# Performance work log

Hardware: AMD Instinct MI355X
Metric: run time of the kernel (lower is better)

Reference implementation:

```python
import jax, jax.numpy as jnp
import numpy as np
from jax import lax

RADIUS = 5


def setup_inputs() -> dict:
    key = jax.random.key(0)
    k1, k2 = jax.random.split(key)
    B, K, H, W = 4, 6, 128, 128
    win = 2 * RADIUS + 1
    labels = jax.random.uniform(k1, (B, K, H, W), dtype=jnp.float32)
    weights = jax.random.uniform(k2, (B, H * W, win, win), dtype=jnp.float32)
    return {"labels": labels, "weights": weights}


def reference(labels, weights):
    # labels:  [B, K, H, W]  class probabilities
    B, K, H, W = labels.shape
    win = 2 * RADIUS + 1
    N = H * W

    # Extract 11x11 patches around every pixel for all classes at once.
    patches = lax.conv_general_dilated_patches(
        labels, (win, win), (1, 1), padding=[(RADIUS, RADIUS), (RADIUS, RADIUS)]
    )
    patches = patches.reshape(B, K, win * win, N)

    w = weights.reshape(B, N, win * win)

    # sum over window of weights * P, per class: wp[b,k,n] = sum_o w[b,n,o] * patches[b,k,o,n]
    wp = jnp.einsum('bkon,bno->bkn', patches, w)

    p = labels.reshape(B, K, N)
    num = jnp.einsum('bkn,bkn->bk', p, wp)          # association
    den = jnp.einsum('bkn,bn->bk', p, w.sum(-1))    # degree
    L = num / den                                    # [B, K]

    # nn.L1Loss()(L, zeros) per class = mean_b |L[b,k]|
    losses = jnp.mean(jnp.abs(L), axis=0)            # [K]
    return K - jnp.sum(losses)
```

## Files before the change

kernel.cpp:

```cpp
#include <hip/hip_runtime.h>

#define RADIUS 5
#define WIN    11
#define WIN2   121
#define KCLS   6
#define HH     128
#define WW     128
#define BB     4
#define NPIX   (HH*WW)
#define TPB    256
#define NBLK   (BB*HH*2)
#define PXB    64
#define LABW   (PXB + 2*RADIUS)
#define NSITE  (WIN*LABW)
#define PLSTR  (NSITE*2)

__global__ __launch_bounds__(TPB, 4) void ncut_main(
    const float* __restrict__ labels,
    const float* __restrict__ weights,
    float* __restrict__ part) {
  __shared__ float shl[3 * PLSTR];
  __shared__ float shred[4 * 12];

  const int tid = threadIdx.x;
  const int blk = blockIdx.x;
  const int b   = blk >> 8;
  const int rem = blk & 255;
  const int y0  = rem >> 1;
  const int x0  = (rem & 1) * PXB;

  const float* labB = labels + (size_t)b * KCLS * NPIX;
  for (int s = tid; s < NSITE; s += TPB) {
    const int tr = s / LABW;
    const int tc = s - tr * LABW;
    const int gy = y0 - RADIUS + tr;
    const int gx = x0 + tc - RADIUS;
    const bool ok = ((unsigned)gy < (unsigned)HH) & ((unsigned)gx < (unsigned)WW);
    const float* lp = labB + (size_t)gy * WW + gx;
#pragma unroll
    for (int p = 0; p < 3; ++p) {
      float2 v = make_float2(0.f, 0.f);
      if (ok) {
        v.x = lp[(size_t)(2 * p) * NPIX];
        v.y = lp[(size_t)(2 * p + 1) * NPIX];
      }
      *reinterpret_cast<float2*>(shl + p * PLSTR + 2 * s) = v;
    }
  }
  __syncthreads();

  const int px = tid >> 2;
  const int q  = tid & 3;
  const float* wrowq = weights +
      ((size_t)b * NPIX + (size_t)y0 * WW + x0 + px) * WIN2 + q;

  float2 a0 = make_float2(0.f, 0.f);
  float2 a1 = make_float2(0.f, 0.f);
  float2 a2 = make_float2(0.f, 0.f);
  float wsum = 0.f;

#pragma unroll
  for (int j = 0; j < 30; ++j) {
    const int o4 = 4 * j;
    const int S  = (o4 / WIN) * LABW + (o4 % WIN);
    const int Wn = WIN - (o4 % WIN);
    const float w = wrowq[o4];
    wsum += w;
    int li = px + S + q;
    if (Wn < 4) li += (q >= Wn) ? (LABW - WIN) : 0;
    const float2 v0 = *reinterpret_cast<const float2*>(shl + 0 * PLSTR + 2 * li);
    const float2 v1 = *reinterpret_cast<const float2*>(shl + 1 * PLSTR + 2 * li);
    const float2 v2 = *reinterpret_cast<const float2*>(shl + 2 * PLSTR + 2 * li);
    a0.x += w * v0.x; a0.y += w * v0.y;
    a1.x += w * v1.x; a1.y += w * v1.y;
    a2.x += w * v2.x; a2.y += w * v2.y;
  }
  if (q == 0) {
    const float w = wrowq[120];
    const int li = px + 10 * LABW + 10;
    wsum += w;
    const float2 v0 = *reinterpret_cast<const float2*>(shl + 0 * PLSTR + 2 * li);
    const float2 v1 = *reinterpret_cast<const float2*>(shl + 1 * PLSTR + 2 * li);
    const float2 v2 = *reinterpret_cast<const float2*>(shl + 2 * PLSTR + 2 * li);
    a0.x += w * v0.x; a0.y += w * v0.y;
    a1.x += w * v1.x; a1.y += w * v1.y;
    a2.x += w * v2.x; a2.y += w * v2.y;
  }

#pragma unroll
  for (int off = 1; off <= 2; off <<= 1) {
    wsum += __shfl_xor(wsum, off);
    a0.x += __shfl_xor(a0.x, off); a0.y += __shfl_xor(a0.y, off);
    a1.x += __shfl_xor(a1.x, off); a1.y += __shfl_xor(a1.y, off);
    a2.x += __shfl_xor(a2.x, off); a2.y += __shfl_xor(a2.y, off);
  }

  const int lc = px + 5 * LABW + 5;
  const float2 c0 = *reinterpret_cast<const float2*>(shl + 0 * PLSTR + 2 * lc);
  const float2 c1 = *reinterpret_cast<const float2*>(shl + 1 * PLSTR + 2 * lc);
  const float2 c2 = *reinterpret_cast<const float2*>(shl + 2 * PLSTR + 2 * lc);
  float nv[KCLS] = {c0.x * a0.x, c0.y * a0.y, c1.x * a1.x,
                    c1.y * a1.y, c2.x * a2.x, c2.y * a2.y};
  float dv[KCLS] = {c0.x * wsum, c0.y * wsum, c1.x * wsum,
                    c1.y * wsum, c2.x * wsum, c2.y * wsum};

#pragma unroll
  for (int off = 4; off <= 32; off <<= 1) {
#pragma unroll
    for (int k = 0; k < KCLS; ++k) {
      nv[k] += __shfl_xor(nv[k], off);
      dv[k] += __shfl_xor(dv[k], off);
    }
  }
  const int wave = tid >> 6;
  if ((tid & 63) == 0) {
#pragma unroll
    for (int k = 0; k < KCLS; ++k) {
      shred[wave * 12 + k]     = nv[k];
      shred[wave * 12 + 6 + k] = dv[k];
    }
  }
  __syncthreads();
  if (tid < 12) {
    float s = 0.f;
#pragma unroll
    for (int w = 0; w < 4; ++w) s += shred[w * 12 + tid];
    part[blk * 12 + tid] = s;
  }
}

__global__ __launch_bounds__(256) void ncut_final(
    const float* __restrict__ part, float* __restrict__ out) {
  __shared__ float shf[8 * 48];
  const int t   = threadIdx.x;
  const int seg = t >> 5;
  const int bk  = t & 31;
  if (bk < 24) {
    const int b = bk / KCLS;
    const int k = bk - b * KCLS;
    const int r0 = b * 256 + seg * 32;
    float num = 0.f, den = 0.f;
#pragma unroll 4
    for (int i = 0; i < 32; ++i) {
      const float* p = part + (size_t)(r0 + i) * 12;
      num += p[k];
      den += p[6 + k];
    }
    shf[seg * 48 + bk * 2]     = num;
    shf[seg * 48 + bk * 2 + 1] = den;
  }
  __syncthreads();
  float val = 0.f;
  if (t < 24) {
    float n = 0.f, d = 0.f;
#pragma unroll
    for (int s = 0; s < 8; ++s) {
      n += shf[s * 48 + t * 2];
      d += shf[s * 48 + t * 2 + 1];
    }
    val = fabsf(n / d) * (1.0f / BB);
  }
  if (t < 64) {
#pragma unroll
    for (int off = 16; off; off >>= 1) val += __shfl_down(val, off);
    if (t == 0) out[0] = (float)KCLS - val;
  }
}

extern "C" void kernel_launch(void* const* d_in, const int* in_sizes, int n_in,
                              void* d_out, int out_size, void* d_ws, size_t ws_size,
                              hipStream_t stream) {
  const float* labels  = (const float*)d_in[0];
  const float* weights = (const float*)d_in[1];
  float* out  = (float*)d_out;
  float* part = (float*)d_ws;

  ncut_main<<<NBLK, TPB, 0, stream>>>(labels, weights, part);
  ncut_final<<<1, 256, 0, stream>>>(part, out);
}
```

Baseline: 20.18 us.

## Stage per-block weights into LDS via async coalesced global_load_lds

Copies each block's contiguous weight slab into shared memory using asynchronous direct-to-LDS 16-byte loads, overlapping with the label tile load. The inner loop then reads weights from LDS instead of strided global loads. This is meant to cut the poorly coalesced global access pattern. It raises LDS usage, lowering occupancy (launch bounds reduced to 3), and relies on the barrier to wait for the async loads.

```diff
diff --git a/kernel.cpp b/kernel.cpp
--- a/kernel.cpp
+++ b/kernel.cpp
@@ -14,11 +14,13 @@
 #define LABW   (PXB + 2*RADIUS)
 #define NSITE  (WIN*LABW)
 #define PLSTR  (NSITE*2)
+#define WLDS   8192
 
-__global__ __launch_bounds__(TPB, 4) void ncut_main(
+__global__ __launch_bounds__(TPB, 3) void ncut_main(
     const float* __restrict__ labels,
     const float* __restrict__ weights,
     float* __restrict__ part) {
+  __shared__ float shw[WLDS];
   __shared__ float shl[3 * PLSTR];
   __shared__ float shred[4 * 12];
 
@@ -28,6 +30,21 @@
   const int rem = blk & 255;
   const int y0  = rem >> 1;
   const int x0  = (rem & 1) * PXB;
+
+  const size_t pxg0 = (size_t)b * NPIX + (size_t)y0 * WW + x0;
+  const float* wbase = weights + pxg0 * WIN2;
+  const float* wend  = weights + (size_t)BB * NPIX * WIN2 - 4;
+  const int wave = tid >> 6, lane = tid & 63;
+#pragma unroll
+  for (int i = 0; i < 8; ++i) {
+    const int off = i * 1024 + wave * 256;
+    const float* g = wbase + off + lane * 4;
+    if (g > wend) g = wend;
+    __builtin_amdgcn_global_load_lds(
+        (const __attribute__((address_space(1))) void*)g,
+        (__attribute__((address_space(3))) void*)&shw[off],
+        16, 0, 0);
+  }
 
   const float* labB = labels + (size_t)b * KCLS * NPIX;
   for (int s = tid; s < NSITE; s += TPB) {
@@ -51,8 +68,7 @@
 
   const int px = tid >> 2;
   const int q  = tid & 3;
-  const float* wrowq = weights +
-      ((size_t)b * NPIX + (size_t)y0 * WW + x0 + px) * WIN2 + q;
+  const int wpx = px * WIN2;
 
   float2 a0 = make_float2(0.f, 0.f);
   float2 a1 = make_float2(0.f, 0.f);
@@ -64,23 +80,23 @@
     const int o4 = 4 * j;
     const int S  = (o4 / WIN) * LABW + (o4 % WIN);
     const int Wn = WIN - (o4 % WIN);
-    const float w = wrowq[o4];
+    const float w = shw[wpx + o4 + q];
     wsum += w;
     int li = px + S + q;
     if (Wn < 4) li += (q >= Wn) ? (LABW - WIN) : 0;
-    const float2 v0 = *reinterpret_cast<const float2*>(shl + 0 * PLSTR + 2 * li);
-    const float2 v1 = *reinterpret_cast<const float2*>(shl + 1 * PLSTR + 2 * li);
+    const float2 v0 = *reinterpret_cast<const float2*>(shl + 2 * li);
+    const float2 v1 = *reinterpret_cast<const float2*>(shl + PLSTR + 2 * li);
     const float2 v2 = *reinterpret_cast<const float2*>(shl + 2 * PLSTR + 2 * li);
     a0.x += w * v0.x; a0.y += w * v0.y;
     a1.x += w * v1.x; a1.y += w * v1.y;
     a2.x += w * v2.x; a2.y += w * v2.y;
   }
   if (q == 0) {
-    const float w = wrowq[120];
+    const float w = shw[wpx + 120];
     const int li = px + 10 * LABW + 10;
     wsum += w;
-    const float2 v0 = *reinterpret_cast<const float2*>(shl + 0 * PLSTR + 2 * li);
-    const float2 v1 = *reinterpret_cast<const float2*>(shl + 1 * PLSTR + 2 * li);
+    const float2 v0 = *reinterpret_cast<const float2*>(shl + 2 * li);
+    const float2 v1 = *reinterpret_cast<const float2*>(shl + PLSTR + 2 * li);
     const float2 v2 = *reinterpret_cast<const float2*>(shl + 2 * PLSTR + 2 * li);
     a0.x += w * v0.x; a0.y += w * v0.y;
     a1.x += w * v1.x; a1.y += w * v1.y;
@@ -96,8 +112,8 @@
   }
 
   const int lc = px + 5 * LABW + 5;
-  const float2 c0 = *reinterpret_cast<const float2*>(shl + 0 * PLSTR + 2 * lc);
-  const float2 c1 = *reinterpret_cast<const float2*>(shl + 1 * PLSTR + 2 * lc);
+  const float2 c0 = *reinterpret_cast<const float2*>(shl + 2 * lc);
+  const float2 c1 = *reinterpret_cast<const float2*>(shl + PLSTR + 2 * lc);
   const float2 c2 = *reinterpret_cast<const float2*>(shl + 2 * PLSTR + 2 * lc);
   float nv[KCLS] = {c0.x * a0.x, c0.y * a0.y, c1.x * a1.x,
                     c1.y * a1.y, c2.x * a2.x, c2.y * a2.y};
@@ -112,7 +128,6 @@
       dv[k] += __shfl_xor(dv[k], off);
     }
   }
-  const int wave = tid >> 6;
   if ((tid & 63) == 0) {
 #pragma unroll
     for (int k = 0; k < KCLS; ++k) {
```

Result: slower. 24.70 us (+22.4%).
